# Kernel tuning notes

Hardware: AMD Instinct MI355X
Metric: run time of the kernel (lower is better)

The kernel has to match this reference:

```python
import jax, jax.numpy as jnp
import numpy as np

EPS = 1e-08
TEMPERATURE = 0.05


def setup_inputs() -> dict:
    key = jax.random.key(0)
    k1, k2 = jax.random.split(key)
    N = 8192
    predict_similarity = jax.random.normal(k1, (N,), dtype=jnp.float32)
    true_similarity = jax.random.uniform(k2, (N,), dtype=jnp.float32)
    return {"predict_similarity": predict_similarity, "true_similarity": true_similarity}


def reference(predict_similarity, true_similarity):
    # Sort descending by ground-truth score
    order = jnp.argsort(-true_similarity)
    yt = true_similarity[order]                      # (N,)
    yp = (predict_similarity / TEMPERATURE)[order]   # (N,)
    N = yt.shape[0]

    # Pairwise ground-truth gaps W[k, j] = yt[k] - yt[j]
    W = yt[:, None] - yt[None, :]                    # (N, N)
    # negatives: strictly later in the sorted order AND strictly lower score
    tri = jnp.triu(jnp.ones((N, N), dtype=bool), 1)
    mask = tri & (W > EPS)
    row_valid = jnp.any(mask, axis=1)                # rows contributing to the loss

    neg_inf = jnp.float32(-jnp.inf)
    # weight for the positive = max gap among its valid negatives
    weight_k = jnp.max(jnp.where(mask, W, neg_inf), axis=1)
    weight_k = jnp.where(row_valid, weight_k, 0.0)

    logit_pos = yp * weight_k                        # (N,)
    L_neg = yp[None, :] * W                          # (N, N) negative logits

    # stable masked logsumexp over {pos} U {masked negatives}
    m = jnp.maximum(logit_pos, jnp.max(jnp.where(mask, L_neg, neg_inf), axis=1))
    m = jnp.where(row_valid, m, 0.0)
    z = jnp.where(mask, L_neg - m[:, None], neg_inf)  # exp(-inf)=0 for masked-out
    sum_exp = jnp.exp(logit_pos - m) + jnp.sum(jnp.exp(z), axis=1)
    log_prob = logit_pos - m - jnp.log(sum_exp)      # log_softmax(...)[0]

    count = jnp.sum(row_valid)
    total = jnp.sum(jnp.where(row_valid, log_prob, 0.0))
    return jnp.where(count > 0, -total / jnp.maximum(count, 1).astype(total.dtype), 0.0)
```

## Files before the change

### kernel.cpp

```cpp
#include <hip/hip_runtime.h>
#include <hip/hip_bf16.h>

#define NN 8192
#define EPSF 1e-8f
#define LOG2E 1.4426950408889634f
#define LN2f 0.6931471805599453f
#define BLOCK 256
#define ROWS 4
#define ROWS_PER_BLOCK (ROWS * (BLOCK / 64))
#define NBLOCKS (NN / ROWS_PER_BLOCK)

#define A2SCALE (20.0f * LOG2E)

__global__ __launch_bounds__(1024) void prep_kernel(const float* __restrict__ yt,
                                                    float* __restrict__ scal) {
    __shared__ float red[16];
    int t = threadIdx.x;
    float mn = INFINITY;
    for (int i = t; i < NN; i += 1024) mn = fminf(mn, yt[i]);
#pragma unroll
    for (int m = 1; m < 64; m <<= 1) mn = fminf(mn, __shfl_xor(mn, m));
    if ((t & 63) == 0) red[t >> 6] = mn;
    __syncthreads();
    if (t < 16) {
        float v = red[t];
#pragma unroll
        for (int m = 1; m < 16; m <<= 1) v = fminf(v, __shfl_xor(v, m));
        if (t == 0) scal[0] = v;
    }
}

__global__ __launch_bounds__(BLOCK) void pro_main(const float* __restrict__ yt_g,
                                                  const float* __restrict__ pred_g,
                                                  const float* __restrict__ scal,
                                                  float* __restrict__ acc) {
    __shared__ float4 yt_s[NN / 4];
    __shared__ float4 a2_s[NN / 4];

    const int t = threadIdx.x;
    const float4* ytg4 = (const float4*)yt_g;
    const float4* pdg4 = (const float4*)pred_g;
    for (int i = t; i < NN / 4; i += BLOCK) {
        yt_s[i] = ytg4[i];
        float4 p = pdg4[i];
        p.x *= A2SCALE; p.y *= A2SCALE; p.z *= A2SCALE; p.w *= A2SCALE;
        a2_s[i] = p;
    }
    __syncthreads();

    const float yt_min = scal[0];
    const int wave = t >> 6, lane = t & 63;
    const int row0 = blockIdx.x * ROWS_PER_BLOCK + wave * ROWS;

    const float* yts = (const float*)yt_s;
    const float* a2s = (const float*)a2_s;

    float x[ROWS], lp[ROWS], M[ROWS], vld[ROWS];
#pragma unroll
    for (int r = 0; r < ROWS; ++r) {
        x[r] = yts[row0 + r];
        float w = x[r] - yt_min;
        vld[r] = (w > EPSF) ? 1.0f : 0.0f;
        lp[r] = a2s[row0 + r] * w;
        M[r] = -INFINITY;
    }

    for (int i = 0; i < NN / 256; ++i) {
        float4 y4 = yt_s[i * 64 + lane];
        float4 a4 = a2_s[i * 64 + lane];
#pragma unroll
        for (int r = 0; r < ROWS; ++r) {
            float W0 = x[r] - y4.x; float L0 = a4.x * W0; M[r] = fmaxf(M[r], (W0 > EPSF) ? L0 : -INFINITY);
            float W1 = x[r] - y4.y; float L1 = a4.y * W1; M[r] = fmaxf(M[r], (W1 > EPSF) ? L1 : -INFINITY);
            float W2 = x[r] - y4.z; float L2 = a4.z * W2; M[r] = fmaxf(M[r], (W2 > EPSF) ? L2 : -INFINITY);
            float W3 = x[r] - y4.w; float L3 = a4.w * W3; M[r] = fmaxf(M[r], (W3 > EPSF) ? L3 : -INFINITY);
        }
    }
#pragma unroll
    for (int r = 0; r < ROWS; ++r) {
#pragma unroll
        for (int m = 1; m < 64; m <<= 1) M[r] = fmaxf(M[r], __shfl_xor(M[r], m));
        M[r] = fmaxf(M[r], lp[r]);
    }

    float s[ROWS];
#pragma unroll
    for (int r = 0; r < ROWS; ++r) s[r] = 0.0f;

    for (int i = 0; i < NN / 256; ++i) {
        float4 y4 = yt_s[i * 64 + lane];
        float4 a4 = a2_s[i * 64 + lane];
#pragma unroll
        for (int r = 0; r < ROWS; ++r) {
            float W0 = x[r] - y4.x; float t0 = __builtin_fmaf(a4.x, W0, -M[r]); s[r] += exp2f((W0 > EPSF) ? t0 : -INFINITY);
            float W1 = x[r] - y4.y; float t1 = __builtin_fmaf(a4.y, W1, -M[r]); s[r] += exp2f((W1 > EPSF) ? t1 : -INFINITY);
            float W2 = x[r] - y4.z; float t2 = __builtin_fmaf(a4.z, W2, -M[r]); s[r] += exp2f((W2 > EPSF) ? t2 : -INFINITY);
            float W3 = x[r] - y4.w; float t3 = __builtin_fmaf(a4.w, W3, -M[r]); s[r] += exp2f((W3 > EPSF) ? t3 : -INFINITY);
        }
    }
#pragma unroll
    for (int r = 0; r < ROWS; ++r) {
#pragma unroll
        for (int m = 1; m < 64; m <<= 1) s[r] += __shfl_xor(s[r], m);
    }

    float wtot = 0.0f, wcnt = 0.0f;
#pragma unroll
    for (int r = 0; r < ROWS; ++r) {
        float lpm = lp[r] - M[r];
        float sum = exp2f(lpm) + s[r];
        float logp = lpm * LN2f - __logf(sum);
        wtot += vld[r] * logp;
        wcnt += vld[r];
    }

    __syncthreads();
    float* wred = (float*)yt_s;
    if (lane == 0) { wred[wave * 2] = wtot; wred[wave * 2 + 1] = wcnt; }
    __syncthreads();
    if (t == 0) {
        float bt = 0.0f, bc = 0.0f;
        for (int w2 = 0; w2 < BLOCK / 64; ++w2) { bt += wred[w2 * 2]; bc += wred[w2 * 2 + 1]; }
        atomicAdd(&acc[0], bt);
        atomicAdd(&acc[1], bc);
    }
}

__global__ void finalize_kernel(const float* __restrict__ acc, float* __restrict__ out) {
    out[0] = (acc[1] > 0.0f) ? (-acc[0] / acc[1]) : 0.0f;
}

extern "C" void kernel_launch(void* const* d_in, const int* in_sizes, int n_in,
                              void* d_out, int out_size, void* d_ws, size_t ws_size,
                              hipStream_t stream) {
    const float* pred = (const float*)d_in[0];
    const float* yt   = (const float*)d_in[1];

    float* scal = (float*)d_ws;
    float* acc  = scal + 1;

    hipMemsetAsync(acc, 0, 2 * sizeof(float), stream);
    prep_kernel<<<1, 1024, 0, stream>>>(yt, scal);
    pro_main<<<NBLOCKS, BLOCK, 0, stream>>>(yt, pred, scal, acc);
    finalize_kernel<<<1, 1, 0, stream>>>(acc, (float*)d_out);
}
```

Before: 97.86 us.

## Split columns into chunks with per-chunk partial logsumexp merged in finalize

The main kernel now splits the 8192 columns into 4 chunks, so each block handles one row group and one chunk. It writes a per-row partial (max, scaled sum) to workspace instead of doing atomics. The yt minimum reduction and the cross-chunk log-sum-exp merge move into a single finalize kernel, which removes the memset and the separate prep launch. This gives 4x more blocks, each with a smaller shared-memory footprint, for better occupancy and parallelism. In exchange it adds workspace traffic and a serial single-block finalize pass over all rows.

```diff
diff --git a/kernel.cpp b/kernel.cpp
--- a/kernel.cpp
+++ b/kernel.cpp
@@ -8,39 +8,25 @@
 #define BLOCK 256
 #define ROWS 4
 #define ROWS_PER_BLOCK (ROWS * (BLOCK / 64))
-#define NBLOCKS (NN / ROWS_PER_BLOCK)
+#define RG (NN / ROWS_PER_BLOCK)
+#define CHUNKS 4
+#define CH (NN / CHUNKS)
 
 #define A2SCALE (20.0f * LOG2E)
 
-__global__ __launch_bounds__(1024) void prep_kernel(const float* __restrict__ yt,
-                                                    float* __restrict__ scal) {
-    __shared__ float red[16];
-    int t = threadIdx.x;
-    float mn = INFINITY;
-    for (int i = t; i < NN; i += 1024) mn = fminf(mn, yt[i]);
-#pragma unroll
-    for (int m = 1; m < 64; m <<= 1) mn = fminf(mn, __shfl_xor(mn, m));
-    if ((t & 63) == 0) red[t >> 6] = mn;
-    __syncthreads();
-    if (t < 16) {
-        float v = red[t];
-#pragma unroll
-        for (int m = 1; m < 16; m <<= 1) v = fminf(v, __shfl_xor(v, m));
-        if (t == 0) scal[0] = v;
-    }
-}
-
 __global__ __launch_bounds__(BLOCK) void pro_main(const float* __restrict__ yt_g,
                                                   const float* __restrict__ pred_g,
-                                                  const float* __restrict__ scal,
-                                                  float* __restrict__ acc) {
-    __shared__ float4 yt_s[NN / 4];
-    __shared__ float4 a2_s[NN / 4];
+                                                  float2* __restrict__ partial) {
+    __shared__ float4 yt_s[CH / 4];
+    __shared__ float4 a2_s[CH / 4];
 
     const int t = threadIdx.x;
-    const float4* ytg4 = (const float4*)yt_g;
-    const float4* pdg4 = (const float4*)pred_g;
-    for (int i = t; i < NN / 4; i += BLOCK) {
+    const int rg = blockIdx.x >> 2;
+    const int c  = blockIdx.x & 3;
+
+    const float4* ytg4 = (const float4*)(yt_g + c * CH);
+    const float4* pdg4 = (const float4*)(pred_g + c * CH);
+    for (int i = t; i < CH / 4; i += BLOCK) {
         yt_s[i] = ytg4[i];
         float4 p = pdg4[i];
         p.x *= A2SCALE; p.y *= A2SCALE; p.z *= A2SCALE; p.w *= A2SCALE;
@@ -48,24 +34,17 @@
     }
     __syncthreads();
 
-    const float yt_min = scal[0];
     const int wave = t >> 6, lane = t & 63;
-    const int row0 = blockIdx.x * ROWS_PER_BLOCK + wave * ROWS;
+    const int row0 = rg * ROWS_PER_BLOCK + wave * ROWS;
 
-    const float* yts = (const float*)yt_s;
-    const float* a2s = (const float*)a2_s;
-
-    float x[ROWS], lp[ROWS], M[ROWS], vld[ROWS];
+    float x[ROWS], M[ROWS];
 #pragma unroll
     for (int r = 0; r < ROWS; ++r) {
-        x[r] = yts[row0 + r];
-        float w = x[r] - yt_min;
-        vld[r] = (w > EPSF) ? 1.0f : 0.0f;
-        lp[r] = a2s[row0 + r] * w;
+        x[r] = yt_g[row0 + r];
         M[r] = -INFINITY;
     }
 
-    for (int i = 0; i < NN / 256; ++i) {
+    for (int i = 0; i < CH / 256; ++i) {
         float4 y4 = yt_s[i * 64 + lane];
         float4 a4 = a2_s[i * 64 + lane];
 #pragma unroll
@@ -80,14 +59,10 @@
     for (int r = 0; r < ROWS; ++r) {
 #pragma unroll
         for (int m = 1; m < 64; m <<= 1) M[r] = fmaxf(M[r], __shfl_xor(M[r], m));
-        M[r] = fmaxf(M[r], lp[r]);
     }
 
-    float s[ROWS];
-#pragma unroll
-    for (int r = 0; r < ROWS; ++r) s[r] = 0.0f;
-
-    for (int i = 0; i < NN / 256; ++i) {
+    float s[ROWS] = {0.f, 0.f, 0.f, 0.f};
+    for (int i = 0; i < CH / 256; ++i) {
         float4 y4 = yt_s[i * 64 + lane];
         float4 a4 = a2_s[i * 64 + lane];
 #pragma unroll
@@ -104,30 +79,63 @@
         for (int m = 1; m < 64; m <<= 1) s[r] += __shfl_xor(s[r], m);
     }
 
-    float wtot = 0.0f, wcnt = 0.0f;
+    if (lane == 0) {
 #pragma unroll
-    for (int r = 0; r < ROWS; ++r) {
-        float lpm = lp[r] - M[r];
-        float sum = exp2f(lpm) + s[r];
-        float logp = lpm * LN2f - __logf(sum);
-        wtot += vld[r] * logp;
-        wcnt += vld[r];
-    }
-
-    __syncthreads();
-    float* wred = (float*)yt_s;
-    if (lane == 0) { wred[wave * 2] = wtot; wred[wave * 2 + 1] = wcnt; }
-    __syncthreads();
-    if (t == 0) {
-        float bt = 0.0f, bc = 0.0f;
-        for (int w2 = 0; w2 < BLOCK / 64; ++w2) { bt += wred[w2 * 2]; bc += wred[w2 * 2 + 1]; }
-        atomicAdd(&acc[0], bt);
-        atomicAdd(&acc[1], bc);
+        for (int r = 0; r < ROWS; ++r) partial[c * NN + row0 + r] = make_float2(M[r], s[r]);
     }
 }
 
-__global__ void finalize_kernel(const float* __restrict__ acc, float* __restrict__ out) {
-    out[0] = (acc[1] > 0.0f) ? (-acc[0] / acc[1]) : 0.0f;
+__global__ __launch_bounds__(1024) void finalize(const float* __restrict__ yt,
+                                                 const float* __restrict__ pred,
+                                                 const float2* __restrict__ partial,
+                                                 float* __restrict__ out) {
+    __shared__ float redm[16];
+    __shared__ float2 red2[16];
+    __shared__ float bmin;
+    const int t = threadIdx.x, lane = t & 63, wave = t >> 6;
+
+    float mn = INFINITY;
+    for (int i = t; i < NN; i += 1024) mn = fminf(mn, yt[i]);
+#pragma unroll
+    for (int m = 1; m < 64; m <<= 1) mn = fminf(mn, __shfl_xor(mn, m));
+    if (lane == 0) redm[wave] = mn;
+    __syncthreads();
+    if (t == 0) {
+        float v = redm[0];
+        for (int i = 1; i < 16; ++i) v = fminf(v, redm[i]);
+        bmin = v;
+    }
+    __syncthreads();
+    const float yt_min = bmin;
+
+    float wtot = 0.f, wcnt = 0.f;
+    for (int row = t; row < NN; row += 1024) {
+        float x = yt[row];
+        float w = x - yt_min;
+        float a2 = pred[row] * A2SCALE;
+        float lp = a2 * w;
+        float2 pc[CHUNKS];
+        float M = lp;
+#pragma unroll
+        for (int c = 0; c < CHUNKS; ++c) {
+            pc[c] = partial[c * NN + row];
+            M = fmaxf(M, pc[c].x);
+        }
+        float sum = exp2f(lp - M);
+#pragma unroll
+        for (int c = 0; c < CHUNKS; ++c) sum += pc[c].y * exp2f(pc[c].x - M);
+        float logp = (lp - M) * LN2f - __logf(sum);
+        if (w > EPSF) { wtot += logp; wcnt += 1.f; }
+    }
+#pragma unroll
+    for (int m = 1; m < 64; m <<= 1) { wtot += __shfl_xor(wtot, m); wcnt += __shfl_xor(wcnt, m); }
+    if (lane == 0) red2[wave] = make_float2(wtot, wcnt);
+    __syncthreads();
+    if (t == 0) {
+        float bt = 0.f, bc = 0.f;
+        for (int i = 0; i < 16; ++i) { bt += red2[i].x; bc += red2[i].y; }
+        out[0] = (bc > 0.f) ? (-bt / bc) : 0.f;
+    }
 }
 
 extern "C" void kernel_launch(void* const* d_in, const int* in_sizes, int n_in,
@@ -136,11 +144,8 @@
     const float* pred = (const float*)d_in[0];
     const float* yt   = (const float*)d_in[1];
 
-    float* scal = (float*)d_ws;
-    float* acc  = scal + 1;
+    float2* partial = (float2*)d_ws;
 
-    hipMemsetAsync(acc, 0, 2 * sizeof(float), stream);
-    prep_kernel<<<1, 1024, 0, stream>>>(yt, scal);
-    pro_main<<<NBLOCKS, BLOCK, 0, stream>>>(yt, pred, scal, acc);
-    finalize_kernel<<<1, 1, 0, stream>>>(acc, (float*)d_out);
+    pro_main<<<RG * CHUNKS, BLOCK, 0, stream>>>(yt, pred, partial);
+    finalize<<<1, 1024, 0, stream>>>(yt, pred, partial, (float*)d_out);
 }
```

Result: faster. 93.02 us (-4.9%).
